# Performance work log

Hardware: AMD Instinct MI355X
Metric: run time of the kernel (lower is better)

## Reference

```python
import jax, jax.numpy as jnp
import numpy as np

N = 100000   # nodes
E = 1600000  # edges (avg degree 16)
H = 4        # heads
D = 32       # per-head dim (= output_dim)
IN = 32      # input_dim (== output_dim for residual)
NEG_SLOPE = 0.2  # DGL GATConv leaky_relu default


def setup_inputs() -> dict:
    key = jax.random.key(0)
    ks = jax.random.split(key, 9)
    h = jax.random.normal(ks[0], (N, IN), jnp.float32)
    src = jax.random.randint(ks[1], (E,), 0, N, jnp.int32)
    dst = jax.random.randint(ks[2], (E,), 0, N, jnp.int32)
    W_fc = jax.random.normal(ks[3], (IN, H * D), jnp.float32) / np.sqrt(IN).astype(np.float32)
    attn_l = jax.random.normal(ks[4], (H, D), jnp.float32) * 0.1
    attn_r = jax.random.normal(ks[5], (H, D), jnp.float32) * 0.1
    bias_gat = jnp.zeros((H * D,), jnp.float32)
    W_out = jax.random.normal(ks[6], (H * D, D), jnp.float32) / np.sqrt(H * D).astype(np.float32)
    b_out = jnp.zeros((D,), jnp.float32)
    return {"h": h, "src": src, "dst": dst, "W_fc": W_fc, "attn_l": attn_l,
            "attn_r": attn_r, "bias_gat": bias_gat, "W_out": W_out, "b_out": b_out}


def reference(h, src, dst, W_fc, attn_l, attn_r, bias_gat, W_out, b_out):
    # GATConv: linear projection to [N, H, D]
    feat = (h @ W_fc).reshape(N, H, D)
    el = jnp.einsum('nhd,hd->nh', feat, attn_l)  # [N,H]
    er = jnp.einsum('nhd,hd->nh', feat, attn_r)  # [N,H]
    # per-edge unnormalized score, leaky relu
    e = el[src] + er[dst]                         # [E,H]
    e = jnp.where(e > 0, e, NEG_SLOPE * e)
    # segment softmax over edges grouped by destination node
    emax = jax.ops.segment_max(e, dst, num_segments=N)            # [N,H]
    ex = jnp.exp(e - emax[dst])                                   # [E,H]
    denom = jax.ops.segment_sum(ex, dst, num_segments=N)         # [N,H]
    alpha = ex / jnp.maximum(denom[dst], 1e-9)                    # [E,H]
    # attention-weighted scatter-add aggregation
    msg = feat[src] * alpha[:, :, None]                           # [E,H,D]
    rst = jax.ops.segment_sum(msg, dst, num_segments=N)          # [N,H,D]
    rst = rst.reshape(N, H * D) + bias_gat
    # out projection + ELU activation + residual
    out = rst @ W_out + b_out
    out = jnp.where(out > 0, out, jnp.expm1(out))  # ELU(alpha=1)
    return h + out
```

## Files before the change

### kernel.cpp

```cpp
#include <hip/hip_runtime.h>
#include <hip/hip_bf16.h>

#define NNODE 100000
#define NEDGE 1600000
#define NBLK_SCAN 98
#define KPH_BLOCKS 1564
#define QINT4 100000
#define FLAGBIT 0x80000000u

static __device__ __forceinline__ uint32_t pack_bf16(float a, float b) {
    __hip_bfloat162 t = __float22bfloat162_rn(make_float2(a, b));
    return *(uint32_t*)&t;
}

__global__ __launch_bounds__(256) void k_proj_hist(
        const float* __restrict__ hin, const float* __restrict__ Wfc,
        const float* __restrict__ attn_l, const float* __restrict__ attn_r,
        uint32_t* __restrict__ feat, float* __restrict__ el, float* __restrict__ er,
        const int* __restrict__ dst, int* __restrict__ cnt, int* __restrict__ pos) {
    int tid = threadIdx.x;
    int ei = blockIdx.x * 256 + tid;
    bool have = ei < NEDGE / 4;
    int4 d, p;
    int* cntp = nullptr;
    if (have) {
        unsigned part = (unsigned)ei / (unsigned)QINT4;
        cntp = cnt + part * NNODE;
        d = ((const int4*)dst)[ei];
        p.x = atomicAdd(&cntp[d.x], 1);
        p.y = atomicAdd(&cntp[d.y], 1);
        p.z = atomicAdd(&cntp[d.z], 1);
        p.w = atomicAdd(&cntp[d.w], 1);
    }
    int l = tid & 63;
    int w = tid >> 6;
    int nbase = blockIdx.x * 64 + w * 16;
    int c0 = l * 2;
    float2 wreg[32];
#pragma unroll
    for (int k = 0; k < 32; k++)
        wreg[k] = *(const float2*)&Wfc[k * 128 + c0];
    float al0 = attn_l[c0], al1 = attn_l[c0 + 1];
    float ar0 = attn_r[c0], ar1 = attn_r[c0 + 1];
#pragma unroll 4
    for (int i = 0; i < 16; i++) {
        int n = nbase + i;
        if (n >= NNODE) break;
        float4 hv[8];
#pragma unroll
        for (int j = 0; j < 8; j++)
            hv[j] = *(const float4*)&hin[n * 32 + j * 4];
        float a0 = 0.f, a1 = 0.f;
#pragma unroll
        for (int j = 0; j < 8; j++) {
            a0 = fmaf(hv[j].x, wreg[j * 4 + 0].x, a0); a1 = fmaf(hv[j].x, wreg[j * 4 + 0].y, a1);
            a0 = fmaf(hv[j].y, wreg[j * 4 + 1].x, a0); a1 = fmaf(hv[j].y, wreg[j * 4 + 1].y, a1);
            a0 = fmaf(hv[j].z, wreg[j * 4 + 2].x, a0); a1 = fmaf(hv[j].z, wreg[j * 4 + 2].y, a1);
            a0 = fmaf(hv[j].w, wreg[j * 4 + 3].x, a0); a1 = fmaf(hv[j].w, wreg[j * 4 + 3].y, a1);
        }
        float ep = a0 * al0 + a1 * al1;
        float rp = a0 * ar0 + a1 * ar1;
#pragma unroll
        for (int m = 8; m; m >>= 1) {
            ep += __shfl_xor(ep, m);
            rp += __shfl_xor(rp, m);
        }
        if ((l & 15) == 0) {
            el[n * 4 + (l >> 4)] = ep;
            er[n * 4 + (l >> 4)] = rp;
        }
        feat[(size_t)n * 64 + l] = pack_bf16(a0, a1);
    }
    if (have) ((int4*)pos)[ei] = p;
}

__global__ __launch_bounds__(256) void k_scan(
        const int* __restrict__ cnt, unsigned* __restrict__ word,
        int* __restrict__ offa, int* __restrict__ pb) {
    __shared__ int s[256];
    __shared__ int sBase;
    int t = threadIdx.x;
    int b = blockIdx.x;
    int base = b * 1024 + t * 4;
    int vA[4], vB[4], vC[4], v[4];
#pragma unroll
    for (int i = 0; i < 4; i++) {
        int n = base + i;
        if (n < NNODE) {
            int a = cnt[n], bb = cnt[NNODE + n], c = cnt[2 * NNODE + n], dd = cnt[3 * NNODE + n];
            vA[i] = a; vB[i] = bb; vC[i] = c;
            v[i] = a + bb + c + dd;
        } else { vA[i] = vB[i] = vC[i] = 0; v[i] = 0; }
    }
    int sum = v[0] + v[1] + v[2] + v[3];
    s[t] = sum;
    __syncthreads();
    for (int d = 1; d < 256; d <<= 1) {
        int x = (t >= d) ? s[t - d] : 0;
        __syncthreads();
        s[t] += x;
        __syncthreads();
    }
    int excl = s[t] - sum;
    if (t == 255)
        __hip_atomic_store(&word[b], (unsigned)s[255] | FLAGBIT,
                           __ATOMIC_RELEASE, __HIP_MEMORY_SCOPE_AGENT);
    if (t < 64) {
        unsigned acc = 0;
        for (int i = t; i < b; i += 64) {
            unsigned wv;
            do {
                wv = __hip_atomic_load(&word[i], __ATOMIC_ACQUIRE, __HIP_MEMORY_SCOPE_AGENT);
            } while (!(wv & FLAGBIT));
            acc += wv & ~FLAGBIT;
        }
#pragma unroll
        for (int o = 32; o; o >>= 1) acc += __shfl_down(acc, o);
        if (t == 0) sBase = (int)acc;
    }
    __syncthreads();
    int o0 = sBase + excl;
#pragma unroll
    for (int i = 0; i < 4; i++) {
        int n = base + i;
        if (n < NNODE) {
            offa[n] = o0;
            pb[n] = o0;
            pb[NNODE + n] = o0 + vA[i];
            pb[2 * NNODE + n] = o0 + vA[i] + vB[i];
            pb[3 * NNODE + n] = o0 + vA[i] + vB[i] + vC[i];
            o0 += v[i];
        }
    }
    if (b == NBLK_SCAN - 1 && t == 255) offa[NNODE] = NEDGE;
}

__global__ __launch_bounds__(256) void k_scatter(const int* __restrict__ src,
                                                 const int* __restrict__ dst,
                                                 const int* __restrict__ pos,
                                                 const int* __restrict__ pb,
                                                 int* __restrict__ ssrc) {
    int i = blockIdx.x * 256 + threadIdx.x;
    if (i >= NEDGE / 4) return;
    unsigned part = (unsigned)i / (unsigned)QINT4;
    const int* pbp = pb + part * NNODE;
    int4 s = ((const int4*)src)[i];
    int4 d = ((const int4*)dst)[i];
    int4 p = ((const int4*)pos)[i];
    int o0 = pbp[d.x];
    int o1 = pbp[d.y];
    int o2 = pbp[d.z];
    int o3 = pbp[d.w];
    ssrc[o0 + p.x] = s.x;
    ssrc[o1 + p.y] = s.y;
    ssrc[o2 + p.z] = s.z;
    ssrc[o3 + p.w] = s.w;
}

#define NPB 4
union SmemU {
    struct { int sS[NPB][64]; float sE[NPB][64][4]; } g;
    struct { float sv[NPB][128]; float sacc[NPB][2][32]; } e;
};

__global__ __launch_bounds__(256) void k_gather(
        const int* __restrict__ off, const int* __restrict__ ssrc,
        const float* __restrict__ el, const float* __restrict__ er,
        const uint32_t* __restrict__ feat, const float* __restrict__ bias_gat,
        const float* __restrict__ Wout, const float* __restrict__ b_out,
        const float* __restrict__ hin, float* __restrict__ out) {
    __shared__ uint32_t sWu[64 * 32];
    __shared__ __align__(16) SmemU U;
    int tid = threadIdx.x;
    for (int i = tid; i < 2048; i += 256) {
        int ccp = i >> 5, j = i & 31;
        sWu[i] = pack_bf16(Wout[(2 * ccp) * 32 + j], Wout[(2 * ccp + 1) * 32 + j]);
    }
    int w = tid >> 6;
    int l = tid & 63;
    int n = blockIdx.x * NPB + w;
    int c0 = l * 2;
    int hh = l >> 4;
    float2 acc = make_float2(0.f, 0.f);
    float den = 0.f;
    int beg = off[n], end = off[n + 1];
    float4 erv = *(const float4*)&er[n * 4];

    for (int base = beg; base < end; base += 64) {
        int cnt = end - base; if (cnt > 64) cnt = 64;
        int s = 0;
        float4 e4 = make_float4(0.f, 0.f, 0.f, 0.f);
        if (l < cnt) {
            s = ssrc[base + l];
            float4 ev = *(const float4*)&el[s * 4];
            e4.x = ev.x + erv.x; e4.x = e4.x > 0.f ? e4.x : 0.2f * e4.x; e4.x = __expf(e4.x);
            e4.y = ev.y + erv.y; e4.y = e4.y > 0.f ? e4.y : 0.2f * e4.y; e4.y = __expf(e4.y);
            e4.z = ev.z + erv.z; e4.z = e4.z > 0.f ? e4.z : 0.2f * e4.z; e4.z = __expf(e4.z);
            e4.w = ev.w + erv.w; e4.w = e4.w > 0.f ? e4.w : 0.2f * e4.w; e4.w = __expf(e4.w);
        }
        U.g.sS[w][l] = s;
        *(float4*)&U.g.sE[w][l][0] = e4;
        __builtin_amdgcn_wave_barrier();
        int rounds = (cnt + 7) >> 3;
        for (int r = 0; r < rounds; r++) {
            int e = r * 8;
            int ss[8]; float xx[8]; uint32_t uu[8];
#pragma unroll
            for (int q = 0; q < 8; q++) {
                ss[q] = U.g.sS[w][e + q];
                xx[q] = U.g.sE[w][e + q][hh];
            }
#pragma unroll
            for (int q = 0; q < 8; q++)
                uu[q] = feat[(uint32_t)ss[q] * 64u + (uint32_t)l];
#pragma unroll
            for (int q = 0; q < 8; q++) {
                den += xx[q];
                acc.x = fmaf(xx[q], __uint_as_float(uu[q] << 16), acc.x);
                acc.y = fmaf(xx[q], __uint_as_float(uu[q] & 0xffff0000u), acc.y);
            }
        }
        __builtin_amdgcn_wave_barrier();
    }
    float inv = 1.f / fmaxf(den, 1e-9f);
    float2 val;
    val.x = acc.x * inv + bias_gat[c0];
    val.y = acc.y * inv + bias_gat[c0 + 1];
    __syncthreads();
    *(float2*)&U.e.sv[w][c0] = val;
    __syncthreads();
    int j = tid & 31, g2 = (l >> 5);
    float p = 0.f;
    const float* vv = U.e.sv[w];
#pragma unroll 8
    for (int ccp = g2 * 32; ccp < g2 * 32 + 32; ccp++) {
        uint32_t u = sWu[ccp * 32 + j];
        p = fmaf(vv[2 * ccp],     __uint_as_float(u << 16),          p);
        p = fmaf(vv[2 * ccp + 1], __uint_as_float(u & 0xffff0000u), p);
    }
    U.e.sacc[w][g2][j] = p;
    __syncthreads();
    if (g2 == 0) {
        float a = U.e.sacc[w][0][j] + U.e.sacc[w][1][j] + b_out[j];
        a = a > 0.f ? a : expm1f(a);
        out[n * 32 + j] = hin[n * 32 + j] + a;
    }
}

extern "C" void kernel_launch(void* const* d_in, const int* in_sizes, int n_in,
                              void* d_out, int out_size, void* d_ws, size_t ws_size,
                              hipStream_t stream) {
    const float* hin      = (const float*)d_in[0];
    const int*   src      = (const int*)d_in[1];
    const int*   dst      = (const int*)d_in[2];
    const float* Wfc      = (const float*)d_in[3];
    const float* attn_l   = (const float*)d_in[4];
    const float* attn_r   = (const float*)d_in[5];
    const float* bias_gat = (const float*)d_in[6];
    const float* Wout     = (const float*)d_in[7];
    const float* b_out    = (const float*)d_in[8];
    float* out = (float*)d_out;

    char* ws = (char*)d_ws;
    size_t o = 0;
    uint32_t* feat = (uint32_t*)(ws + o); o += (size_t)NNODE * 64 * 4;
    float* el      = (float*)(ws + o);    o += (size_t)NNODE * 4 * 4;
    float* er      = (float*)(ws + o);    o += (size_t)NNODE * 4 * 4;
    int*   cnt     = (int*)(ws + o);      o += (size_t)4 * NNODE * 4;
    unsigned* word = (unsigned*)(ws + o); o += (size_t)NBLK_SCAN * 4;
    int*   offa    = (int*)(ws + o);      o += (size_t)(NNODE + 1) * 4;
    int*   pb      = (int*)(ws + o);      o += (size_t)4 * NNODE * 4;
    int*   pos     = (int*)(ws + o);      o += (size_t)NEDGE * 4;
    int*   ssrc    = (int*)(ws + o);      o += (size_t)NEDGE * 4;

    hipMemsetAsync(cnt, 0, (size_t)(4 * NNODE + NBLK_SCAN) * 4, stream);

    k_proj_hist<<<KPH_BLOCKS, 256, 0, stream>>>(
        hin, Wfc, attn_l, attn_r, feat, el, er, dst, cnt, pos);
    k_scan<<<NBLK_SCAN, 256, 0, stream>>>(cnt, word, offa, pb);
    k_scatter<<<(NEDGE / 4 + 255) / 256, 256, 0, stream>>>(src, dst, pos, pb, ssrc);
    k_gather<<<NNODE / NPB, 256, 0, stream>>>(offa, ssrc, el, er, feat, bias_gat,
                                              Wout, b_out, hin, out);
}
```

Baseline: 222.6 us.

## Split output projection out of gather kernel into separate k_out kernel

Moves the W_out projection, ELU and residual out of the per-node gather kernel into a new kernel that handles 32 nodes per block. The gather kernel now writes the normalized aggregated features as bf16 to a workspace buffer. This drops the per-block staging of W_out, the extra syncthreads and the large shared-memory union from the gather kernel, which is meant to improve its occupancy. In exchange it adds a kernel launch and a round trip of the 25.6MB intermediate through global memory.

```diff
diff --git a/kernel.cpp b/kernel.cpp
--- a/kernel.cpp
+++ b/kernel.cpp
@@ -158,24 +158,14 @@
 }
 
 #define NPB 4
-union SmemU {
-    struct { int sS[NPB][64]; float sE[NPB][64][4]; } g;
-    struct { float sv[NPB][128]; float sacc[NPB][2][32]; } e;
-};
-
 __global__ __launch_bounds__(256) void k_gather(
         const int* __restrict__ off, const int* __restrict__ ssrc,
         const float* __restrict__ el, const float* __restrict__ er,
         const uint32_t* __restrict__ feat, const float* __restrict__ bias_gat,
-        const float* __restrict__ Wout, const float* __restrict__ b_out,
-        const float* __restrict__ hin, float* __restrict__ out) {
-    __shared__ uint32_t sWu[64 * 32];
-    __shared__ __align__(16) SmemU U;
+        uint32_t* __restrict__ svb) {
+    __shared__ int sS[NPB][64];
+    __shared__ __align__(16) float sE[NPB][64][4];
     int tid = threadIdx.x;
-    for (int i = tid; i < 2048; i += 256) {
-        int ccp = i >> 5, j = i & 31;
-        sWu[i] = pack_bf16(Wout[(2 * ccp) * 32 + j], Wout[(2 * ccp + 1) * 32 + j]);
-    }
     int w = tid >> 6;
     int l = tid & 63;
     int n = blockIdx.x * NPB + w;
@@ -198,8 +188,8 @@
             e4.z = ev.z + erv.z; e4.z = e4.z > 0.f ? e4.z : 0.2f * e4.z; e4.z = __expf(e4.z);
             e4.w = ev.w + erv.w; e4.w = e4.w > 0.f ? e4.w : 0.2f * e4.w; e4.w = __expf(e4.w);
         }
-        U.g.sS[w][l] = s;
-        *(float4*)&U.g.sE[w][l][0] = e4;
+        sS[w][l] = s;
+        *(float4*)&sE[w][l][0] = e4;
         __builtin_amdgcn_wave_barrier();
         int rounds = (cnt + 7) >> 3;
         for (int r = 0; r < rounds; r++) {
@@ -207,8 +197,8 @@
             int ss[8]; float xx[8]; uint32_t uu[8];
 #pragma unroll
             for (int q = 0; q < 8; q++) {
-                ss[q] = U.g.sS[w][e + q];
-                xx[q] = U.g.sE[w][e + q][hh];
+                ss[q] = sS[w][e + q];
+                xx[q] = sE[w][e + q][hh];
             }
 #pragma unroll
             for (int q = 0; q < 8; q++)
@@ -223,26 +213,41 @@
         __builtin_amdgcn_wave_barrier();
     }
     float inv = 1.f / fmaxf(den, 1e-9f);
-    float2 val;
-    val.x = acc.x * inv + bias_gat[c0];
-    val.y = acc.y * inv + bias_gat[c0 + 1];
+    float a0 = acc.x * inv + bias_gat[c0];
+    float a1 = acc.y * inv + bias_gat[c0 + 1];
+    svb[(size_t)n * 64 + l] = pack_bf16(a0, a1);
+}
+
+#define ONPB 32
+__global__ __launch_bounds__(256) void k_out(
+        const uint32_t* __restrict__ svb, const float* __restrict__ Wout,
+        const float* __restrict__ b_out, const float* __restrict__ hin,
+        float* __restrict__ out) {
+    __shared__ float sW[128 * 32];
+    __shared__ uint32_t sV[ONPB * 64];
+    int tid = threadIdx.x;
+    for (int i = tid * 4; i < 4096; i += 1024)
+        *(float4*)&sW[i] = *(const float4*)&Wout[i];
+    for (int i = tid * 8; i < ONPB * 64; i += 2048) {
+        *(uint4*)&sV[i]     = *(const uint4*)&svb[(size_t)blockIdx.x * ONPB * 64 + i];
+        *(uint4*)&sV[i + 4] = *(const uint4*)&svb[(size_t)blockIdx.x * ONPB * 64 + i + 4];
+    }
     __syncthreads();
-    *(float2*)&U.e.sv[w][c0] = val;
-    __syncthreads();
-    int j = tid & 31, g2 = (l >> 5);
-    float p = 0.f;
-    const float* vv = U.e.sv[w];
-#pragma unroll 8
-    for (int ccp = g2 * 32; ccp < g2 * 32 + 32; ccp++) {
-        uint32_t u = sWu[ccp * 32 + j];
-        p = fmaf(vv[2 * ccp],     __uint_as_float(u << 16),          p);
-        p = fmaf(vv[2 * ccp + 1], __uint_as_float(u & 0xffff0000u), p);
-    }
-    U.e.sacc[w][g2][j] = p;
-    __syncthreads();
-    if (g2 == 0) {
-        float a = U.e.sacc[w][0][j] + U.e.sacc[w][1][j] + b_out[j];
-        a = a > 0.f ? a : expm1f(a);
+    int j = tid & 31, ng = tid >> 5;
+    float bj = b_out[j];
+#pragma unroll
+    for (int s = 0; s < 4; s++) {
+        int nl = ng * 4 + s;
+        int n = blockIdx.x * ONPB + nl;
+        float p = bj;
+        const uint32_t* vv = &sV[nl * 64];
+#pragma unroll 16
+        for (int ccp = 0; ccp < 64; ccp++) {
+            uint32_t u = vv[ccp];
+            p = fmaf(__uint_as_float(u << 16),         sW[(2 * ccp) * 32 + j],     p);
+            p = fmaf(__uint_as_float(u & 0xffff0000u), sW[(2 * ccp + 1) * 32 + j], p);
+        }
+        float a = p > 0.f ? p : expm1f(p);
         out[n * 32 + j] = hin[n * 32 + j] + a;
     }
 }
@@ -264,6 +269,7 @@
     char* ws = (char*)d_ws;
     size_t o = 0;
     uint32_t* feat = (uint32_t*)(ws + o); o += (size_t)NNODE * 64 * 4;
+    uint32_t* svb  = (uint32_t*)(ws + o); o += (size_t)NNODE * 64 * 4;
     float* el      = (float*)(ws + o);    o += (size_t)NNODE * 4 * 4;
     float* er      = (float*)(ws + o);    o += (size_t)NNODE * 4 * 4;
     int*   cnt     = (int*)(ws + o);      o += (size_t)4 * NNODE * 4;
@@ -279,6 +285,6 @@
         hin, Wfc, attn_l, attn_r, feat, el, er, dst, cnt, pos);
     k_scan<<<NBLK_SCAN, 256, 0, stream>>>(cnt, word, offa, pb);
     k_scatter<<<(NEDGE / 4 + 255) / 256, 256, 0, stream>>>(src, dst, pos, pb, ssrc);
-    k_gather<<<NNODE / NPB, 256, 0, stream>>>(offa, ssrc, el, er, feat, bias_gat,
-                                              Wout, b_out, hin, out);
-}
+    k_gather<<<NNODE / NPB, 256, 0, stream>>>(offa, ssrc, el, er, feat, bias_gat, svb);
+    k_out<<<NNODE / ONPB, 256, 0, stream>>>(svb, Wout, b_out, hin, out);
+}
```

Result: slower. 236.0 us (+6.0%).
